# Kernel optimization log

Measured on AMD Instinct MI355X. Metric: run time of the kernel, lower is better.

The kernel has to match this reference:

```python
import jax, jax.numpy as jnp
import numpy as np
from jax import lax

B = 128
NODES = 304
T_STEPS = 20
HID = 64
GCN_IN = 20
N = B * NODES            # 38912 graph nodes
E = N * 16               # 622592 edges
BN_EPS = 1e-5


def setup_inputs() -> dict:
    key = jax.random.key(0)
    ks = jax.random.split(key, 32)
    rn = lambda k, s, sc=0.1: jax.random.normal(k, s, jnp.float32) * sc
    return {
        "data_x": jax.random.normal(ks[0], (N, GCN_IN), jnp.float32),
        "edge_index": jax.random.randint(ks[1], (2, E), 0, N),
        "edge_weight": jax.random.uniform(ks[2], (E,), jnp.float32),
        "tc1_w1": rn(ks[3], (HID, 1, 1, 3)), "tc1_b1": rn(ks[4], (HID,)),
        "tc1_w2": rn(ks[5], (HID, 1, 1, 3)), "tc1_b2": rn(ks[6], (HID,)),
        "tc1_w3": rn(ks[7], (HID, 1, 1, 3)), "tc1_b3": rn(ks[8], (HID,)),
        "gcn_W0": rn(ks[9], (GCN_IN, HID)), "gcn_b0": rn(ks[10], (HID,)),
        "bn0_g": jax.random.uniform(ks[11], (HID,), jnp.float32, 0.5, 1.5), "bn0_b": rn(ks[12], (HID,)),
        "gcn_W1": rn(ks[13], (HID, HID)), "gcn_b1": rn(ks[14], (HID,)),
        "bn1_g": jax.random.uniform(ks[15], (HID,), jnp.float32, 0.5, 1.5), "bn1_b": rn(ks[16], (HID,)),
        "tc2_w1": rn(ks[17], (1, HID, 1, 3)), "tc2_b1": rn(ks[18], (1,)),
        "tc2_w2": rn(ks[19], (1, HID, 1, 3)), "tc2_b2": rn(ks[20], (1,)),
        "tc2_w3": rn(ks[21], (1, HID, 1, 3)), "tc2_b3": rn(ks[22], (1,)),
        "bn2d_g": jax.random.uniform(ks[23], (NODES,), jnp.float32, 0.5, 1.5), "bn2d_b": rn(ks[24], (NODES,)),
        "fc_W": rn(ks[25], (21 * NODES, 2048), 0.01), "fc_b": rn(ks[26], (2048,)),
        "fc4_W": rn(ks[27], (2048, 300), 0.01), "fc4_b": rn(ks[28], (300,)),
    }


def _bn(x, g, b):
    # eval-mode BatchNorm with fresh running stats (mean=0, var=1)
    return x * (g / jnp.sqrt(1.0 + BN_EPS)) + b


def _temporal_conv(X, w1, b1, w2, b2, w3, b3):
    # X: [B, T, nodes, C] -> permute to NCHW [B, C, nodes, T]
    Xp = jnp.transpose(X, (0, 3, 2, 1))
    conv = lambda w, b: lax.conv_general_dilated(
        Xp, w, (1, 1), [(0, 0), (1, 1)],
        dimension_numbers=("NCHW", "OIHW", "NCHW")) + b[None, :, None, None]
    P = conv(w1, b1)
    Q = jax.nn.sigmoid(conv(w2, b2))
    H = jax.nn.relu(P * Q + conv(w3, b3))
    return jnp.transpose(H, (0, 3, 2, 1))  # back to [B, T, nodes, C_out]


def reference(data_x, edge_index, edge_weight,
              tc1_w1, tc1_b1, tc1_w2, tc1_b2, tc1_w3, tc1_b3,
              gcn_W0, gcn_b0, bn0_g, bn0_b,
              gcn_W1, gcn_b1, bn1_g, bn1_b,
              tc2_w1, tc2_b1, tc2_w2, tc2_b2, tc2_w3, tc2_b3,
              bn2d_g, bn2d_b, fc_W, fc_b, fc4_W, fc4_b):
    n = data_x.shape[0]
    b = n // NODES

    # ---- GCN norm (sym, self-loops w=1) ----
    row, col = edge_index[0], edge_index[1]
    loop = jnp.arange(n)
    rowF = jnp.concatenate([row, loop])
    colF = jnp.concatenate([col, loop])
    ewF = jnp.concatenate([edge_weight, jnp.ones((n,), data_x.dtype)])
    deg = jax.ops.segment_sum(ewF, colF, num_segments=n)
    dinv = lax.rsqrt(jnp.maximum(deg, 1e-12))
    norm = dinv[rowF] * ewF * dinv[colF]

    def gconv(x, W, bias):
        h = x @ W
        return jax.ops.segment_sum(h[rowF] * norm[:, None], colF, num_segments=n) + bias

    x = jax.nn.relu(_bn(gconv(data_x, gcn_W0, gcn_b0), bn0_g, bn0_b))
    x = jax.nn.relu(_bn(gconv(x, gcn_W1, gcn_b1), bn1_g, bn1_b))  # [N, HID]

    # ---- temporal conv 1 ----
    X = data_x.reshape(b, T_STEPS, NODES, 1)
    T0 = _temporal_conv(X, tc1_w1, tc1_b1, tc1_w2, tc1_b2, tc1_w3, tc1_b3)  # [B,20,304,HID]

    # gcn_feature.permute(1,0).reshape(-1, 1, nodes, HID)
    gfeat = x.T.reshape(b, 1, NODES, HID)

    T = jnp.concatenate([jax.nn.relu(T0), gfeat], axis=1)  # [B, 21, 304, HID]
    T = jax.nn.relu(T)

    # ---- temporal conv 2 ----
    T = _temporal_conv(T, tc2_w1, tc2_b1, tc2_w2, tc2_b2, tc2_w3, tc2_b3)  # [B,21,304,1]

    # BatchNorm2d over node channel (axis=2 here), eval-mode running stats
    T = T * (bn2d_g / jnp.sqrt(1.0 + BN_EPS))[None, None, :, None] + bn2d_b[None, None, :, None]

    T = T.reshape(b, -1)  # [B, 6384]
    T = jax.nn.relu(T @ fc_W + fc_b)
    return T @ fc4_W + fc4_b  # [B, 300]
```

## Files before the change

### kernel.cpp

```cpp
#include <hip/hip_runtime.h>

#define NODES   304
#define BATCH   128
#define TSTEPS  20
#define HID     64
#define GCNIN   20
#define NN      (BATCH*NODES)
#define NE      (NN*16)
#define SEGSZ   (NN/4)
#define BCAP    64
#define FC1_IN  (21*NODES)
#define KP1     6400
#define FC1_OUT 2048
#define FC2_OUT 300
#define NP2     304
#define BN_EPS  1e-5f

typedef __attribute__((ext_vector_type(8))) short short8;
typedef __attribute__((ext_vector_type(4))) float f32x4;
typedef __attribute__((ext_vector_type(2))) float f32x2;

static __device__ __forceinline__ short f2bf(float x) {
    unsigned u = __float_as_uint(x);
    unsigned r = (u + 0x7FFF + ((u >> 16) & 1)) >> 16;
    return (short)r;
}
static __device__ __forceinline__ float bf2f(unsigned short v) {
    return __uint_as_float((unsigned)v << 16);
}

static __device__ __forceinline__ float fast_sigmoid(float q) {
    return __builtin_amdgcn_rcpf(1.f + __expf(-q));
}

static __device__ __forceinline__ f32x2 pk_fma(f32x2 a, f32x2 b, f32x2 c) {
    f32x2 d;
    asm("v_pk_fma_f32 %0, %1, %2, %3" : "=v"(d) : "v"(a), "v"(b), "v"(c));
    return d;
}

template <int C>
static __device__ __forceinline__ float dppadd(float v) {
    return v + __int_as_float(
        __builtin_amdgcn_update_dpp(0, __float_as_int(v), C, 0xF, 0xF, false));
}
static __device__ __forceinline__ float rsum16(float v) {
    v = dppadd<0x128>(v);
    v = dppadd<0x124>(v);
    v = dppadd<0x122>(v);
    v = dppadd<0x121>(v);
    return v;
}

__global__ void k_bucket(const int* __restrict__ ei, const float* __restrict__ ew,
                         int* __restrict__ cnt, int2* __restrict__ bucket) {
    int e = blockIdx.x * blockDim.x + threadIdx.x;
    if (e < NE) {
        int c = ei[NE + e];
        int slot = atomicAdd(&cnt[c], 1);
        if (slot < BCAP) {
            int2 v;
            v.x = ei[e];
            v.y = __float_as_int(ew[e]);
            bucket[((size_t)c << 6) + slot] = v;
        }
    }
}

__global__ __launch_bounds__(256) void k_dinv2(const int* __restrict__ cnt,
                                               const int2* __restrict__ bucket,
                                               float* __restrict__ dinv) {
    int c = blockIdx.x * 256 + threadIdx.x;
    if (c >= NN) return;
    int n = cnt[c];
    if (n > BCAP) n = BCAP;
    const int2* bp = bucket + ((size_t)c << 6);
    float s = 1.f;
    for (int i = 0; i < n; i += 8) {
        float v[8];
#pragma unroll
        for (int k = 0; k < 8; k++) {
            int l = (i + k < n) ? i + k : n - 1;
            v[k] = (i + k < n) ? __int_as_float(bp[l].y) : 0.f;
        }
#pragma unroll
        for (int k = 0; k < 8; k++) s += v[k];
    }
    dinv[c] = rsqrtf(fmaxf(s, 1e-12f));
}

__global__ __launch_bounds__(256) void k_mm20(const float* __restrict__ X,
                                              const float* __restrict__ W,
                                              const float* __restrict__ dinv,
                                              unsigned short* __restrict__ H) {
    int wv = threadIdx.x >> 6, f = threadIdx.x & 63;
    int n = blockIdx.x * 4 + wv;
    __shared__ float xs[4][GCNIN];
    if (f < GCNIN) xs[wv][f] = X[(size_t)n * GCNIN + f];
    __syncthreads();
    float acc = 0.f;
#pragma unroll
    for (int k = 0; k < GCNIN; k++) acc = fmaf(xs[wv][k], W[k * HID + f], acc);
    H[(size_t)n * HID + f] = (unsigned short)f2bf(acc * dinv[n]);
}

static __device__ __forceinline__ void stage_partition(
    const int* __restrict__ cnt, const int2* __restrict__ bucket, int c, int f,
    int wv, int (*sIdx)[BCAP], float (*sWt)[BCAP], int& dcap) {
    int deg = cnt[c];
    dcap = deg < BCAP ? deg : BCAP;
    bool valid = f < dcap;
    int row = 0;
    float w = 0.f;
    if (valid) {
        int2 e = bucket[((size_t)c << 6) + f];
        row = e.x;
        w = __int_as_float(e.y);
    }
    int q = (row >= SEGSZ) + (row >= 2 * SEGSZ) + (row >= 3 * SEGSZ);
    unsigned long long b0 = __ballot(valid && q == 0);
    unsigned long long b1 = __ballot(valid && q == 1);
    unsigned long long b2 = __ballot(valid && q == 2);
    unsigned long long b3 = __ballot(valid && q == 3);
    unsigned long long lmask = (1ULL << f) - 1;
    int pos = 0;
    if (q > 0) pos += __popcll(b0);
    if (q > 1) pos += __popcll(b1);
    if (q > 2) pos += __popcll(b2);
    unsigned long long mybal = (q == 0) ? b0 : (q == 1) ? b1 : (q == 2) ? b2 : b3;
    pos += __popcll(mybal & lmask);
    if (valid) {
        sIdx[wv][pos] = row;
        sWt[wv][pos] = w;
    }
}

__global__ __launch_bounds__(256) void k_gatherA(const int* __restrict__ cnt,
                                                 const int2* __restrict__ bucket,
                                                 const float* __restrict__ dinv,
                                                 const unsigned short* __restrict__ H0,
                                                 const float* __restrict__ gb,
                                                 const float* __restrict__ bng,
                                                 const float* __restrict__ bnb,
                                                 const float* __restrict__ W1,
                                                 unsigned short* __restrict__ H1) {
    int wv = threadIdx.x >> 6, f = threadIdx.x & 63;
    int c = blockIdx.x * 4 + wv;
    __shared__ int sIdx[4][BCAP];
    __shared__ float sWt[4][BCAP];
    __shared__ float xs[4][HID];

    int dcap;
    stage_partition(cnt, bucket, c, f, wv, sIdx, sWt, dcap);
    __syncthreads();

    float dc = dinv[c];
    float acc = bf2f(H0[(size_t)c * HID + f]);
    for (int base = 0; base < dcap; base += 16) {
        int idx[16];
        float w[16];
#pragma unroll
        for (int i = 0; i < 16; i++) {
            int l = (base + i < dcap) ? base + i : dcap - 1;
            idx[i] = sIdx[wv][l];
            w[i] = (base + i < dcap) ? sWt[wv][l] : 0.f;
        }
        float v[16];
#pragma unroll
        for (int i = 0; i < 16; i++) v[i] = bf2f(H0[(size_t)idx[i] * HID + f]);
#pragma unroll
        for (int i = 0; i < 16; i++) acc = fmaf(v[i], w[i], acc);
    }
    float scale = bng[f] * rsqrtf(1.f + BN_EPS);
    float y = fmaxf(fmaf(acc * dc + gb[f], scale, bnb[f]), 0.f);

    xs[wv][f] = y;
    __syncthreads();
    float h = 0.f;
#pragma unroll
    for (int k4 = 0; k4 < HID / 4; k4++) {
        float4 xv = *(const float4*)&xs[wv][k4 * 4];
        h = fmaf(xv.x, W1[(k4 * 4 + 0) * HID + f], h);
        h = fmaf(xv.y, W1[(k4 * 4 + 1) * HID + f], h);
        h = fmaf(xv.z, W1[(k4 * 4 + 2) * HID + f], h);
        h = fmaf(xv.w, W1[(k4 * 4 + 3) * HID + f], h);
    }
    H1[(size_t)c * HID + f] = (unsigned short)f2bf(h * dc);
}

__global__ __launch_bounds__(256) void k_gatherB(const int* __restrict__ cnt,
                                                 const int2* __restrict__ bucket,
                                                 const float* __restrict__ dinv,
                                                 const unsigned short* __restrict__ H,
                                                 const float* __restrict__ gb,
                                                 const float* __restrict__ bng,
                                                 const float* __restrict__ bnb,
                                                 float* __restrict__ XO) {
    int wv = threadIdx.x >> 6, f = threadIdx.x & 63;
    int c = blockIdx.x * 4 + wv;
    __shared__ int sIdx[4][BCAP];
    __shared__ float sWt[4][BCAP];

    int dcap;
    stage_partition(cnt, bucket, c, f, wv, sIdx, sWt, dcap);
    __syncthreads();

    float dc = dinv[c];
    float acc = bf2f(H[(size_t)c * HID + f]);
    for (int base = 0; base < dcap; base += 16) {
        int idx[16];
        float w[16];
#pragma unroll
        for (int i = 0; i < 16; i++) {
            int l = (base + i < dcap) ? base + i : dcap - 1;
            idx[i] = sIdx[wv][l];
            w[i] = (base + i < dcap) ? sWt[wv][l] : 0.f;
        }
        float v[16];
#pragma unroll
        for (int i = 0; i < 16; i++) v[i] = bf2f(H[(size_t)idx[i] * HID + f]);
#pragma unroll
        for (int i = 0; i < 16; i++) acc = fmaf(v[i], w[i], acc);
    }
    float scale = bng[f] * rsqrtf(1.f + BN_EPS);
    XO[(size_t)c * HID + f] = fmaxf(fmaf(acc * dc + gb[f], scale, bnb[f]), 0.f);
}

__global__ __launch_bounds__(256) void k_xpose(const float* __restrict__ x2,
                                               float* __restrict__ x2t) {
    __shared__ float tile[64][65];
    int n0 = blockIdx.x * 64;
    for (int i = threadIdx.x; i < 4096; i += 256) {
        int r = i >> 6, h = i & 63;
        tile[r][h] = x2[(size_t)(n0 + r) * 64 + h];
    }
    __syncthreads();
    for (int i = threadIdx.x; i < 4096; i += 256) {
        int h = i >> 6, c = i & 63;
        x2t[(size_t)h * NN + n0 + c] = tile[c][h];
    }
}

__global__ __launch_bounds__(256) void k_temporal2(
    const float* __restrict__ data_x, const float* __restrict__ x2t,
    const float* __restrict__ w1, const float* __restrict__ b1,
    const float* __restrict__ w2, const float* __restrict__ b2,
    const float* __restrict__ w3, const float* __restrict__ b3,
    const float* __restrict__ v1, const float* __restrict__ vb1,
    const float* __restrict__ v2, const float* __restrict__ vb2,
    const float* __restrict__ v3, const float* __restrict__ vb3,
    const float* __restrict__ bn2g, const float* __restrict__ bn2b,
    short* __restrict__ Ab) {
    int bn0 = blockIdx.x * 16;
    int b = bn0 / NODES, node0 = bn0 % NODES;
    int tid = threadIdx.x;
    int p = tid >> 4;
    int c0 = (tid & 15) << 2;
    int node = node0 + p;

    __shared__ float xs[16][22];
    for (int i = tid; i < 320; i += 256) {
        int t = i >> 4, pp = i & 15;
        xs[pp][t + 1] = data_x[b * (TSTEPS * NODES) + t * NODES + node0 + pp];
    }
    if (tid < 16) { xs[tid][0] = 0.f; xs[tid][21] = 0.f; }

    f32x2 A1p[2][3], A2p[2][3], A3p[2][3], B1p[2], B2p[2], B3p[2];
    f32x2 U1p[2][3], U2p[2][3], U3p[2][3];
#pragma unroll
    for (int cp = 0; cp < 2; cp++) {
        int ca = c0 + 2 * cp, cb = ca + 1;
#pragma unroll
        for (int k = 0; k < 3; k++) {
            A1p[cp][k][0] = w1[ca * 3 + k]; A1p[cp][k][1] = w1[cb * 3 + k];
            A2p[cp][k][0] = w2[ca * 3 + k]; A2p[cp][k][1] = w2[cb * 3 + k];
            A3p[cp][k][0] = w3[ca * 3 + k]; A3p[cp][k][1] = w3[cb * 3 + k];
            U1p[cp][k][0] = v1[ca * 3 + k]; U1p[cp][k][1] = v1[cb * 3 + k];
            U2p[cp][k][0] = v2[ca * 3 + k]; U2p[cp][k][1] = v2[cb * 3 + k];
            U3p[cp][k][0] = v3[ca * 3 + k]; U3p[cp][k][1] = v3[cb * 3 + k];
        }
        B1p[cp][0] = b1[ca]; B1p[cp][1] = b1[cb];
        B2p[cp][0] = b2[ca]; B2p[cp][1] = b2[cb];
        B3p[cp][0] = b3[ca]; B3p[cp][1] = b3[cb];
    }
    float cb1 = vb1[0], cb2 = vb2[0], cb3 = vb3[0];
    float s2 = bn2g[node] * rsqrtf(1.f + BN_EPS);
    float bb2 = bn2b[node];
    short* dst = Ab + (size_t)b * KP1;

    __syncthreads();

    f32x2 hA2[2] = {}, hB2[2] = {}, hC2[2];
    float xr0 = xs[p][0], xr1 = xs[p][1];

#pragma unroll
    for (int j = 0; j <= 21; j++) {
        if (j < 20) {
            float xr2 = xs[p][j + 2];
            f32x2 x0d, x1d, x2d;
            x0d[0] = xr0; x0d[1] = xr0;
            x1d[0] = xr1; x1d[1] = xr1;
            x2d[0] = xr2; x2d[1] = xr2;
#pragma unroll
            for (int cp = 0; cp < 2; cp++) {
                f32x2 pv = pk_fma(A1p[cp][2], x2d,
                            pk_fma(A1p[cp][1], x1d, pk_fma(A1p[cp][0], x0d, B1p[cp])));
                f32x2 qv = pk_fma(A2p[cp][2], x2d,
                            pk_fma(A2p[cp][1], x1d, pk_fma(A2p[cp][0], x0d, B2p[cp])));
                f32x2 rv = pk_fma(A3p[cp][2], x2d,
                            pk_fma(A3p[cp][1], x1d, pk_fma(A3p[cp][0], x0d, B3p[cp])));
                hC2[cp][0] = fmaxf(fmaf(pv[0], fast_sigmoid(qv[0]), rv[0]), 0.f);
                hC2[cp][1] = fmaxf(fmaf(pv[1], fast_sigmoid(qv[1]), rv[1]), 0.f);
            }
            xr0 = xr1;
            xr1 = xr2;
        } else if (j == 20) {
            const float4 gv = *(const float4*)(x2t + (size_t)(b >> 1) * NN +
                                               (b & 1) * (NODES * HID) + node * HID + c0);
            hC2[0][0] = fmaxf(gv.x, 0.f);
            hC2[0][1] = fmaxf(gv.y, 0.f);
            hC2[1][0] = fmaxf(gv.z, 0.f);
            hC2[1][1] = fmaxf(gv.w, 0.f);
        } else {
            hC2[0][0] = 0.f; hC2[0][1] = 0.f;
            hC2[1][0] = 0.f; hC2[1][1] = 0.f;
        }
        if (j >= 1) {
            int w = j - 1;
            f32x2 pa, qa, ra;
            pa[0] = 0.f; pa[1] = 0.f;
            qa[0] = 0.f; qa[1] = 0.f;
            ra[0] = 0.f; ra[1] = 0.f;
#pragma unroll
            for (int cp = 0; cp < 2; cp++) {
                pa = pk_fma(U1p[cp][0], hA2[cp], pa);
                pa = pk_fma(U1p[cp][1], hB2[cp], pa);
                pa = pk_fma(U1p[cp][2], hC2[cp], pa);
                qa = pk_fma(U2p[cp][0], hA2[cp], qa);
                qa = pk_fma(U2p[cp][1], hB2[cp], qa);
                qa = pk_fma(U2p[cp][2], hC2[cp], qa);
                ra = pk_fma(U3p[cp][0], hA2[cp], ra);
                ra = pk_fma(U3p[cp][1], hB2[cp], ra);
                ra = pk_fma(U3p[cp][2], hC2[cp], ra);
            }
            float pp_ = rsum16(pa[0] + pa[1]);
            float qq_ = rsum16(qa[0] + qa[1]);
            float rr_ = rsum16(ra[0] + ra[1]);
            float P = pp_ + cb1, Q = qq_ + cb2, R = rr_ + cb3;
            float hv = fmaxf(fmaf(P, fast_sigmoid(Q), R), 0.f);
            if ((tid & 15) == 0) dst[w * NODES + node] = f2bf(fmaf(hv, s2, bb2));
        }
        hA2[0] = hB2[0]; hA2[1] = hB2[1];
        hB2[0] = hC2[0]; hB2[1] = hC2[1];
    }
}

__global__ __launch_bounds__(256) void k_cvtW4(const float* __restrict__ W,
                                               short* __restrict__ Wt) {
    __shared__ float t[32][33];
    int tx = threadIdx.x & 31, ty = threadIdx.x >> 5;
    int n0 = blockIdx.x * 32, k0 = blockIdx.y * 32;
#pragma unroll
    for (int r = 0; r < 32; r += 8) {
        int k = k0 + r + ty, n = n0 + tx;
        t[r + ty][tx] = (n < FC2_OUT) ? W[(size_t)k * FC2_OUT + n] : 0.f;
    }
    __syncthreads();
#pragma unroll
    for (int r = 0; r < 32; r += 8) {
        int n = n0 + r + ty;
        if (n < NP2) Wt[(size_t)n * FC1_OUT + k0 + tx] = f2bf(t[tx][r + ty]);
    }
}

#define KSPL1 8
#define KCH1  (KP1 / KSPL1)
__global__ __launch_bounds__(256) void k_gemm1f(const short* __restrict__ Ab,
                                                const float* __restrict__ fcW,
                                                float* __restrict__ part) {
    int lane = threadIdx.x & 63, wv = threadIdx.x >> 6;
    int r = lane & 15, kg = lane >> 4;
    int nb = blockIdx.x * 64, sp = blockIdx.y;

    f32x4 acc[2][4] = {};
    const short* a0 = Ab + (size_t)(wv * 32 + r) * KP1;
    const short* a1 = a0 + (size_t)16 * KP1;

    int k0 = sp * KCH1 + kg * 8;
    const float* wp = fcW + (size_t)k0 * FC1_OUT + nb + r;
    bool tailblk = (sp == KSPL1 - 1);

#pragma unroll 1
    for (int s = 0; s < KCH1 / 32; s++, k0 += 32) {
        short8 av0 = *(const short8*)(a0 + k0);
        short8 av1 = *(const short8*)(a1 + k0);
        short8 bv[4];
        if (tailblk && s == KCH1 / 32 - 1) {
#pragma unroll
            for (int f = 0; f < 4; f++)
#pragma unroll
                for (int i = 0; i < 8; i++) {
                    float v = (k0 + i < FC1_IN) ? wp[(size_t)i * FC1_OUT + f * 16] : 0.f;
                    bv[f][i] = f2bf(v);
                }
        } else {
#pragma unroll
            for (int f = 0; f < 4; f++)
#pragma unroll
                for (int i = 0; i < 8; i++)
                    bv[f][i] = f2bf(wp[(size_t)i * FC1_OUT + f * 16]);
        }
        acc[0][0] = __builtin_amdgcn_mfma_f32_16x16x32_bf16(av0, bv[0], acc[0][0], 0, 0, 0);
        acc[1][0] = __builtin_amdgcn_mfma_f32_16x16x32_bf16(av1, bv[0], acc[1][0], 0, 0, 0);
        acc[0][1] = __builtin_amdgcn_mfma_f32_16x16x32_bf16(av0, bv[1], acc[0][1], 0, 0, 0);
        acc[1][1] = __builtin_amdgcn_mfma_f32_16x16x32_bf16(av1, bv[1], acc[1][1], 0, 0, 0);
        acc[0][2] = __builtin_amdgcn_mfma_f32_16x16x32_bf16(av0, bv[2], acc[0][2], 0, 0, 0);
        acc[1][2] = __builtin_amdgcn_mfma_f32_16x16x32_bf16(av1, bv[2], acc[1][2], 0, 0, 0);
        acc[0][3] = __builtin_amdgcn_mfma_f32_16x16x32_bf16(av0, bv[3], acc[0][3], 0, 0, 0);
        acc[1][3] = __builtin_amdgcn_mfma_f32_16x16x32_bf16(av1, bv[3], acc[1][3], 0, 0, 0);
        wp += (size_t)32 * FC1_OUT;
    }

    float* dst = part + (size_t)sp * BATCH * FC1_OUT;
#pragma unroll
    for (int m = 0; m < 2; m++)
#pragma unroll
        for (int f = 0; f < 4; f++)
#pragma unroll
            for (int j = 0; j < 4; j++) {
                int row = wv * 32 + m * 16 + kg * 4 + j;
                int col = nb + f * 16 + r;
                dst[(size_t)row * FC1_OUT + col] = acc[m][f][j];
            }
}

__global__ __launch_bounds__(256) void k_reduce1(const float* __restrict__ part,
                                                 const float* __restrict__ bias,
                                                 short* __restrict__ Ab2) {
    int idx = blockIdx.x * 256 + threadIdx.x;
    int o = idx & (FC1_OUT - 1);
    float s = bias[o];
#pragma unroll
    for (int sp = 0; sp < KSPL1; sp++) s += part[(size_t)sp * BATCH * FC1_OUT + idx];
    Ab2[idx] = f2bf(fmaxf(s, 0.f));
}

#define KSPL2 8
#define KCH2  (FC1_OUT / KSPL2)
__global__ __launch_bounds__(256) void k_gemm2(const short* __restrict__ Ab,
                                               const short* __restrict__ Wt,
                                               float* __restrict__ part) {
    int lane = threadIdx.x & 63, wv = threadIdx.x >> 6;
    int r = lane & 15, kg = lane >> 4;
    int nb = blockIdx.x * 16, sp = blockIdx.y;

    f32x4 acc[2] = {};
    const short* a0 = Ab + (size_t)(wv * 32 + r) * FC1_OUT;
    const short* a1 = a0 + (size_t)16 * FC1_OUT;
    const short* bp = Wt + (size_t)(nb + r) * FC1_OUT;

    int k0 = sp * KCH2 + kg * 8;
#pragma unroll
    for (int s = 0; s < KCH2 / 32; s++, k0 += 32) {
        short8 av0 = *(const short8*)(a0 + k0);
        short8 av1 = *(const short8*)(a1 + k0);
        short8 bv = *(const short8*)(bp + k0);
        acc[0] = __builtin_amdgcn_mfma_f32_16x16x32_bf16(av0, bv, acc[0], 0, 0, 0);
        acc[1] = __builtin_amdgcn_mfma_f32_16x16x32_bf16(av1, bv, acc[1], 0, 0, 0);
    }

    float* dst = part + (size_t)sp * BATCH * NP2;
#pragma unroll
    for (int m = 0; m < 2; m++)
#pragma unroll
        for (int j = 0; j < 4; j++) {
            int row = wv * 32 + m * 16 + kg * 4 + j;
            int col = nb + r;
            dst[(size_t)row * NP2 + col] = acc[m][j];
        }
}

__global__ __launch_bounds__(256) void k_reduce2(const float* __restrict__ part,
                                                 const float* __restrict__ bias,
                                                 float* __restrict__ out) {
    int idx = blockIdx.x * 256 + threadIdx.x;
    if (idx >= BATCH * NP2) return;
    int b = idx / NP2, o = idx % NP2;
    float s = 0.f;
#pragma unroll
    for (int sp = 0; sp < KSPL2; sp++) s += part[(size_t)sp * BATCH * NP2 + idx];
    if (o < FC2_OUT) out[(size_t)b * FC2_OUT + o] = s + bias[o];
}

extern "C" void kernel_launch(void* const* d_in, const int* in_sizes, int n_in,
                              void* d_out, int out_size, void* d_ws, size_t ws_size,
                              hipStream_t stream) {
    const float* data_x = (const float*)d_in[0];
    const int* ei = (const int*)d_in[1];
    const float* ew = (const float*)d_in[2];
    const float* tc1w1 = (const float*)d_in[3];
    const float* tc1b1 = (const float*)d_in[4];
    const float* tc1w2 = (const float*)d_in[5];
    const float* tc1b2 = (const float*)d_in[6];
    const float* tc1w3 = (const float*)d_in[7];
    const float* tc1b3 = (const float*)d_in[8];
    const float* W0 = (const float*)d_in[9];
    const float* gb0 = (const float*)d_in[10];
    const float* bn0g = (const float*)d_in[11];
    const float* bn0b = (const float*)d_in[12];
    const float* W1 = (const float*)d_in[13];
    const float* gb1 = (const float*)d_in[14];
    const float* bn1g = (const float*)d_in[15];
    const float* bn1b = (const float*)d_in[16];
    const float* tc2w1 = (const float*)d_in[17];
    const float* tc2b1 = (const float*)d_in[18];
    const float* tc2w2 = (const float*)d_in[19];
    const float* tc2b2 = (const float*)d_in[20];
    const float* tc2w3 = (const float*)d_in[21];
    const float* tc2b3 = (const float*)d_in[22];
    const float* bn2g = (const float*)d_in[23];
    const float* bn2b = (const float*)d_in[24];
    const float* fcW = (const float*)d_in[25];
    const float* fcb = (const float*)d_in[26];
    const float* fc4W = (const float*)d_in[27];
    const float* fc4b = (const float*)d_in[28];
    float* out = (float*)d_out;

    char* ws = (char*)d_ws;
    float* x2 = (float*)(ws + 0);
    short* Ab = (short*)(ws + 9961472);
    const size_t ARENA = 9961472 + 1638400;

    size_t off = ARENA;
    auto alloc = [&](size_t bytes) -> void* {
        void* p = ws + off;
        off = (off + bytes + 255) & ~(size_t)255;
        return p;
    };
    int2* bucket = (int2*)alloc((size_t)NN * BCAP * 8);
    int* cnt = (int*)alloc((size_t)NN * 4);
    float* dinv = (float*)alloc((size_t)NN * 4);
    unsigned short* h0 = (unsigned short*)alloc((size_t)NN * HID * 2);
    unsigned short* h1 = (unsigned short*)alloc((size_t)NN * HID * 2);

    float* x2t = (float*)(ws + ARENA);

    off = ARENA;
    float* part1 = (float*)alloc((size_t)KSPL1 * BATCH * FC1_OUT * 4);
    short* Ab2 = (short*)alloc((size_t)BATCH * FC1_OUT * 2);
    short* W4t = (short*)alloc((size_t)NP2 * FC1_OUT * 2);
    float* part2 = (float*)alloc((size_t)KSPL2 * BATCH * NP2 * 4);
    (void)ws_size; (void)in_sizes; (void)n_in; (void)out_size;

    hipMemsetAsync(cnt, 0, (size_t)NN * 4, stream);
    k_bucket<<<(NE + 255) / 256, 256, 0, stream>>>(ei, ew, cnt, bucket);
    k_dinv2<<<(NN + 255) / 256, 256, 0, stream>>>(cnt, bucket, dinv);

    k_mm20<<<NN / 4, 256, 0, stream>>>(data_x, W0, dinv, h0);
    k_gatherA<<<NN / 4, 256, 0, stream>>>(cnt, bucket, dinv, h0, gb0, bn0g, bn0b,
                                          W1, h1);
    k_gatherB<<<NN / 4, 256, 0, stream>>>(cnt, bucket, dinv, h1, gb1, bn1g, bn1b, x2);

    k_xpose<<<NN / 64, 256, 0, stream>>>(x2, x2t);

    hipMemsetAsync(Ab, 0, (size_t)BATCH * KP1 * 2, stream);
    k_temporal2<<<NN / 16, 256, 0, stream>>>(data_x, x2t, tc1w1, tc1b1, tc1w2, tc1b2,
                                             tc1w3, tc1b3, tc2w1, tc2b1, tc2w2, tc2b2,
                                             tc2w3, tc2b3, bn2g, bn2b, Ab);

    {
        dim3 g(FC1_OUT / 64, KSPL1);
        k_gemm1f<<<g, 256, 0, stream>>>(Ab, fcW, part1);
    }
    k_reduce1<<<BATCH * FC1_OUT / 256, 256, 0, stream>>>(part1, fcb, Ab2);
    {
        dim3 g((NP2 + 31) / 32, FC1_OUT / 32);
        k_cvtW4<<<g, 256, 0, stream>>>(fc4W, W4t);
    }
    {
        dim3 g(NP2 / 16, KSPL2);
        k_gemm2<<<g, 256, 0, stream>>>(Ab2, W4t, part2);
    }
    k_reduce2<<<(BATCH * NP2 + 255) / 256, 256, 0, stream>>>(part2, fc4b, out);
}
```

Before: 214.7 us.

## Fuse degree normalization into mm20, hoist gather loads, stage temporal weights in LDS

```diff
diff --git a/kernel.cpp b/kernel.cpp
--- a/kernel.cpp
+++ b/kernel.cpp
@@ -67,56 +67,44 @@
     }
 }
 
-__global__ __launch_bounds__(256) void k_dinv2(const int* __restrict__ cnt,
-                                               const int2* __restrict__ bucket,
-                                               float* __restrict__ dinv) {
-    int c = blockIdx.x * 256 + threadIdx.x;
-    if (c >= NN) return;
-    int n = cnt[c];
-    if (n > BCAP) n = BCAP;
-    const int2* bp = bucket + ((size_t)c << 6);
-    float s = 1.f;
-    for (int i = 0; i < n; i += 8) {
-        float v[8];
-#pragma unroll
-        for (int k = 0; k < 8; k++) {
-            int l = (i + k < n) ? i + k : n - 1;
-            v[k] = (i + k < n) ? __int_as_float(bp[l].y) : 0.f;
-        }
-#pragma unroll
-        for (int k = 0; k < 8; k++) s += v[k];
-    }
-    dinv[c] = rsqrtf(fmaxf(s, 1e-12f));
-}
-
 __global__ __launch_bounds__(256) void k_mm20(const float* __restrict__ X,
                                               const float* __restrict__ W,
-                                              const float* __restrict__ dinv,
-                                              unsigned short* __restrict__ H) {
+                                              const int* __restrict__ cnt,
+                                              const int2* __restrict__ bucket,
+                                              unsigned short* __restrict__ H,
+                                              float* __restrict__ dinv) {
     int wv = threadIdx.x >> 6, f = threadIdx.x & 63;
     int n = blockIdx.x * 4 + wv;
     __shared__ float xs[4][GCNIN];
+    __shared__ float rs[4][4];
+
+    int2 be = bucket[((size_t)n << 6) + f];
+    int deg = cnt[n];
     if (f < GCNIN) xs[wv][f] = X[(size_t)n * GCNIN + f];
+
+    int dcap = deg < BCAP ? deg : BCAP;
+    float wsum = (f < dcap) ? __int_as_float(be.y) : 0.f;
+    wsum = rsum16(wsum);
+    if ((f & 15) == 0) rs[wv][f >> 4] = wsum;
     __syncthreads();
+
+    float dv = rsqrtf(fmaxf(1.f + rs[wv][0] + rs[wv][1] + rs[wv][2] + rs[wv][3],
+                            1e-12f));
+    if (f == 0) dinv[n] = dv;
+
     float acc = 0.f;
 #pragma unroll
     for (int k = 0; k < GCNIN; k++) acc = fmaf(xs[wv][k], W[k * HID + f], acc);
-    H[(size_t)n * HID + f] = (unsigned short)f2bf(acc * dinv[n]);
+    H[(size_t)n * HID + f] = (unsigned short)f2bf(acc * dv);
 }
 
 static __device__ __forceinline__ void stage_partition(
-    const int* __restrict__ cnt, const int2* __restrict__ bucket, int c, int f,
-    int wv, int (*sIdx)[BCAP], float (*sWt)[BCAP], int& dcap) {
-    int deg = cnt[c];
+    int deg, int2 e, int f, int wv, int (*sIdx)[BCAP], float (*sWt)[BCAP],
+    int& dcap) {
     dcap = deg < BCAP ? deg : BCAP;
     bool valid = f < dcap;
-    int row = 0;
-    float w = 0.f;
-    if (valid) {
-        int2 e = bucket[((size_t)c << 6) + f];
-        row = e.x;
-        w = __int_as_float(e.y);
-    }
+    int row = e.x;
+    float w = __int_as_float(e.y);
     int q = (row >= SEGSZ) + (row >= 2 * SEGSZ) + (row >= 3 * SEGSZ);
     unsigned long long b0 = __ballot(valid && q == 0);
     unsigned long long b1 = __ballot(valid && q == 1);
@@ -150,12 +138,16 @@
     __shared__ float sWt[4][BCAP];
     __shared__ float xs[4][HID];
 
+    int2 be = bucket[((size_t)c << 6) + f];
+    int deg = cnt[c];
+    float dc = dinv[c];
+    float self = bf2f(H0[(size_t)c * HID + f]);
+
     int dcap;
-    stage_partition(cnt, bucket, c, f, wv, sIdx, sWt, dcap);
+    stage_partition(deg, be, f, wv, sIdx, sWt, dcap);
     __syncthreads();
 
-    float dc = dinv[c];
-    float acc = bf2f(H0[(size_t)c * HID + f]);
+    float acc = self;
     for (int base = 0; base < dcap; base += 16) {
         int idx[16];
         float w[16];
@@ -201,12 +193,16 @@
     __shared__ int sIdx[4][BCAP];
     __shared__ float sWt[4][BCAP];
 
+    int2 be = bucket[((size_t)c << 6) + f];
+    int deg = cnt[c];
+    float dc = dinv[c];
+    float self = bf2f(H[(size_t)c * HID + f]);
+
     int dcap;
-    stage_partition(cnt, bucket, c, f, wv, sIdx, sWt, dcap);
+    stage_partition(deg, be, f, wv, sIdx, sWt, dcap);
     __syncthreads();
 
-    float dc = dinv[c];
-    float acc = bf2f(H[(size_t)c * HID + f]);
+    float acc = self;
     for (int base = 0; base < dcap; base += 16) {
         int idx[16];
         float w[16];
@@ -239,6 +235,18 @@
         int h = i >> 6, c = i & 63;
         x2t[(size_t)h * NN + n0 + c] = tile[c][h];
     }
+}
+
+static __device__ __forceinline__ void load12(const float* base, f32x2 P[2][3]) {
+    float4 f0 = *(const float4*)(base);
+    float4 f1 = *(const float4*)(base + 4);
+    float4 f2 = *(const float4*)(base + 8);
+    P[0][0][0] = f0.x; P[0][0][1] = f0.w;
+    P[0][1][0] = f0.y; P[0][1][1] = f1.x;
+    P[0][2][0] = f0.z; P[0][2][1] = f1.y;
+    P[1][0][0] = f1.z; P[1][0][1] = f2.y;
+    P[1][1][0] = f1.w; P[1][1][1] = f2.z;
+    P[1][2][0] = f2.x; P[1][2][1] = f2.w;
 }
 
 __global__ __launch_bounds__(256) void k_temporal2(
@@ -259,36 +267,50 @@
     int node = node0 + p;
 
     __shared__ float xs[16][22];
+    __shared__ float wlds[1344];
+
+    if (tid < 192) {
+        wlds[tid] = w1[tid];
+        wlds[192 + tid] = w2[tid];
+        wlds[384 + tid] = w3[tid];
+        wlds[576 + tid] = v1[tid];
+        wlds[768 + tid] = v2[tid];
+        wlds[960 + tid] = v3[tid];
+    }
+    if (tid < 64) {
+        wlds[1152 + tid] = b1[tid];
+        wlds[1216 + tid] = b2[tid];
+        wlds[1280 + tid] = b3[tid];
+    }
     for (int i = tid; i < 320; i += 256) {
         int t = i >> 4, pp = i & 15;
         xs[pp][t + 1] = data_x[b * (TSTEPS * NODES) + t * NODES + node0 + pp];
     }
     if (tid < 16) { xs[tid][0] = 0.f; xs[tid][21] = 0.f; }
 
-    f32x2 A1p[2][3], A2p[2][3], A3p[2][3], B1p[2], B2p[2], B3p[2];
-    f32x2 U1p[2][3], U2p[2][3], U3p[2][3];
-#pragma unroll
-    for (int cp = 0; cp < 2; cp++) {
-        int ca = c0 + 2 * cp, cb = ca + 1;
-#pragma unroll
-        for (int k = 0; k < 3; k++) {
-            A1p[cp][k][0] = w1[ca * 3 + k]; A1p[cp][k][1] = w1[cb * 3 + k];
-            A2p[cp][k][0] = w2[ca * 3 + k]; A2p[cp][k][1] = w2[cb * 3 + k];
-            A3p[cp][k][0] = w3[ca * 3 + k]; A3p[cp][k][1] = w3[cb * 3 + k];
-            U1p[cp][k][0] = v1[ca * 3 + k]; U1p[cp][k][1] = v1[cb * 3 + k];
-            U2p[cp][k][0] = v2[ca * 3 + k]; U2p[cp][k][1] = v2[cb * 3 + k];
-            U3p[cp][k][0] = v3[ca * 3 + k]; U3p[cp][k][1] = v3[cb * 3 + k];
-        }
-        B1p[cp][0] = b1[ca]; B1p[cp][1] = b1[cb];
-        B2p[cp][0] = b2[ca]; B2p[cp][1] = b2[cb];
-        B3p[cp][0] = b3[ca]; B3p[cp][1] = b3[cb];
-    }
     float cb1 = vb1[0], cb2 = vb2[0], cb3 = vb3[0];
     float s2 = bn2g[node] * rsqrtf(1.f + BN_EPS);
     float bb2 = bn2b[node];
     short* dst = Ab + (size_t)b * KP1;
 
     __syncthreads();
+
+    f32x2 A1p[2][3], A2p[2][3], A3p[2][3], B1p[2], B2p[2], B3p[2];
+    f32x2 U1p[2][3], U2p[2][3], U3p[2][3];
+    load12(&wlds[0 + c0 * 3], A1p);
+    load12(&wlds[192 + c0 * 3], A2p);
+    load12(&wlds[384 + c0 * 3], A3p);
+    load12(&wlds[576 + c0 * 3], U1p);
+    load12(&wlds[768 + c0 * 3], U2p);
+    load12(&wlds[960 + c0 * 3], U3p);
+    {
+        float4 t1 = *(const float4*)&wlds[1152 + c0];
+        float4 t2 = *(const float4*)&wlds[1216 + c0];
+        float4 t3 = *(const float4*)&wlds[1280 + c0];
+        B1p[0][0] = t1.x; B1p[0][1] = t1.y; B1p[1][0] = t1.z; B1p[1][1] = t1.w;
+        B2p[0][0] = t2.x; B2p[0][1] = t2.y; B2p[1][0] = t2.z; B2p[1][1] = t2.w;
+        B3p[0][0] = t3.x; B3p[0][1] = t3.y; B3p[1][0] = t3.z; B3p[1][1] = t3.w;
+    }
 
     f32x2 hA2[2] = {}, hB2[2] = {}, hC2[2];
     float xr0 = xs[p][0], xr1 = xs[p][1];
@@ -554,9 +576,8 @@
 
     hipMemsetAsync(cnt, 0, (size_t)NN * 4, stream);
     k_bucket<<<(NE + 255) / 256, 256, 0, stream>>>(ei, ew, cnt, bucket);
-    k_dinv2<<<(NN + 255) / 256, 256, 0, stream>>>(cnt, bucket, dinv);
-
-    k_mm20<<<NN / 4, 256, 0, stream>>>(data_x, W0, dinv, h0);
+
+    k_mm20<<<NN / 4, 256, 0, stream>>>(data_x, W0, cnt, bucket, h0, dinv);
     k_gatherA<<<NN / 4, 256, 0, stream>>>(cnt, bucket, dinv, h0, gb0, bn0g, bn0b,
                                           W1, h1);
     k_gatherB<<<NN / 4, 256, 0, stream>>>(cnt, bucket, dinv, h1, gb1, bn1g, bn1b, x2);
```

Result: faster. 205.7 us (-4.2%).
